# Kernel tuning notes

Measured on AMD Instinct MI355X. Metric: run time of the kernel, lower is better.

Reference implementation:

```python
import jax, jax.numpy as jnp
import numpy as np
import math

DIMS = 128
VOXEL_SIZE = 4.0
QUANT_SIZE = 0.02
QUANT_LEN = int((2 * VOXEL_SIZE + 0.0001) // QUANT_SIZE)  # 400
N = 1024


def setup_inputs() -> dict:
    key = jax.random.key(0)
    k1, k2, k3, k4, k5, k6 = jax.random.split(key, 6)
    features = jax.random.normal(k1, (N, DIMS), dtype=jnp.float32)
    # distances uniform in [-voxel_size, voxel_size)
    voxel_distances = (jax.random.uniform(k2, (N, N, 3), dtype=jnp.float32) * 2.0 - 1.0) * VOXEL_SIZE
    W_qkv = jax.random.normal(k3, (DIMS, 3 * DIMS), dtype=jnp.float32) * 0.02
    b_qkv = jnp.zeros((3 * DIMS,), dtype=jnp.float32)
    table_x = jax.random.normal(k4, (3, QUANT_LEN, DIMS), dtype=jnp.float32) * 0.02
    table_y = jax.random.normal(k5, (3, QUANT_LEN, DIMS), dtype=jnp.float32) * 0.02
    table_z = jax.random.normal(k6, (3, QUANT_LEN, DIMS), dtype=jnp.float32) * 0.02
    return {"features": features, "voxel_distances": voxel_distances,
            "W_qkv": W_qkv, "b_qkv": b_qkv,
            "table_x": table_x, "table_y": table_y, "table_z": table_z}


def reference(features, voxel_distances, W_qkv, b_qkv, table_x, table_y, table_z):
    n, dims = features.shape
    qkv = (features @ W_qkv + b_qkv).reshape(n, 3, dims)
    q, k, v = qkv[:, 0], qkv[:, 1], qkv[:, 2]  # each [N, D]

    # quantized distance indices, clamped like torch's .clamp(max=...)
    max_idx = VOXEL_SIZE * 2.0 / QUANT_SIZE - 1.0  # 399
    idx = jnp.floor((voxel_distances + VOXEL_SIZE) / QUANT_SIZE)
    idx = jnp.clip(idx, 0.0, max_idx).astype(jnp.int32)  # [N, N, 3]

    # gathered positional encoding: [N, N, D]
    encode_k = table_x[1][idx[:, :, 0]] + table_y[1][idx[:, :, 1]] + table_z[1][idx[:, :, 2]]
    # bias[i, j] = k[i] . encode_k[i, j]  (faithful to k[:, None] @ encode_k^T)
    position_bias = jnp.einsum('id,ijd->ij', k, encode_k)

    scores = (q @ k.T + position_bias) / math.sqrt(dims)
    attn = jax.nn.softmax(scores, axis=-1)  # [N, N]
    return attn @ v  # [N, D]
```

## Files before the change

### kernel.cpp

```cpp
#include <hip/hip_runtime.h>
#include <math.h>

#define N_PTS 1024
#define D 128
#define QL 400
#define PLD 1200
#define SQRT_D_INV 0.08838834764831845f

typedef __attribute__((ext_vector_type(8))) short bf16x8;
typedef __attribute__((ext_vector_type(4))) float f32x4;
typedef unsigned short u16;

#define GLOBAL_AS __attribute__((address_space(1)))
#define LDS_AS    __attribute__((address_space(3)))

__device__ __forceinline__ u16 f2bf(float x) {
    union { float f; unsigned u; } v; v.f = x;
    unsigned r = v.u + 0x7fff + ((v.u >> 16) & 1);
    return (u16)(r >> 16);
}
__device__ __forceinline__ float b2f(u16 h) {
    union { unsigned u; float f; } v; v.u = ((unsigned)h) << 16;
    return v.f;
}

__global__ __launch_bounds__(256) void prep_kernel(
    const float* __restrict__ features, const float* __restrict__ W,
    const float* __restrict__ bias,
    const float* __restrict__ tx, const float* __restrict__ ty,
    const float* __restrict__ tz,
    u16* __restrict__ qb, u16* __restrict__ kb, u16* __restrict__ vT,
    u16* __restrict__ Tcat)
{
    __shared__ __align__(16) u16 As[64 * 128];
    __shared__ __align__(16) u16 Bs[64 * 128];
    const int tid = threadIdx.x;
    const int bx = blockIdx.x;

    if (bx >= 96) {
        int e0 = (bx - 96) * 1024 + tid * 4;
        int n = e0 >> 7, k = e0 & 127;
        int sec = n / QL, r = n - sec * QL;
        const float* t = (sec == 0) ? tx : ((sec == 1) ? ty : tz);
        float4 v = *(const float4*)&t[QL * D + r * D + k];
        ushort4 o;
        o.x = f2bf(v.x); o.y = f2bf(v.y); o.z = f2bf(v.z); o.w = f2bf(v.w);
        *(ushort4*)&Tcat[e0] = o;
        return;
    }

    const int wave = tid >> 6, lane = tid & 63;
    const int wr = wave >> 1, wc = wave & 1;
    const int l15 = lane & 15, l4 = lane >> 4;
    const int bm = (bx / 6) * 64;
    const int bn = (bx % 6) * 64;

    #pragma unroll
    for (int r0 = 0; r0 < 4; ++r0) {
        int unit = r0 * 256 + tid;
        int row = unit >> 4, c16 = unit & 15;
        const float* ga = features + (size_t)(bm + row) * D + c16 * 8;
        float4 a0 = *(const float4*)ga;
        float4 a1 = *(const float4*)(ga + 4);
        u16 h[8] = {f2bf(a0.x), f2bf(a0.y), f2bf(a0.z), f2bf(a0.w),
                    f2bf(a1.x), f2bf(a1.y), f2bf(a1.z), f2bf(a1.w)};
        *(bf16x8*)(As + row * 128 + ((c16 ^ (row & 7)) * 8)) = *(bf16x8*)h;
    }
    #pragma unroll
    for (int r2 = 0; r2 < 8; ++r2) {
        int k = r2 * 16 + (tid >> 4);
        int nl = (tid & 15) * 4;
        float4 w4 = *(const float4*)&W[(size_t)k * 384 + bn + nl];
        float wv[4] = {w4.x, w4.y, w4.z, w4.w};
        #pragma unroll
        for (int e = 0; e < 4; ++e) {
            int n = nl + e;
            Bs[n * 128 + ((k >> 3) ^ (n & 7)) * 8 + (k & 7)] = f2bf(wv[e]);
        }
    }
    __syncthreads();

    f32x4 acc[2][2] = {};
    #pragma unroll
    for (int ks = 0; ks < 4; ++ks) {
        bf16x8 a[2], b[2];
        #pragma unroll
        for (int m = 0; m < 2; ++m) {
            int row = wr * 32 + m * 16 + l15;
            int c16 = ks * 4 + l4;
            a[m] = *(const bf16x8*)(As + row * 128 + ((c16 ^ (row & 7)) * 8));
        }
        #pragma unroll
        for (int n = 0; n < 2; ++n) {
            int row = wc * 32 + n * 16 + l15;
            int c16 = ks * 4 + l4;
            b[n] = *(const bf16x8*)(Bs + row * 128 + ((c16 ^ (row & 7)) * 8));
        }
        #pragma unroll
        for (int m = 0; m < 2; ++m)
            #pragma unroll
            for (int n = 0; n < 2; ++n)
                acc[m][n] = __builtin_amdgcn_mfma_f32_16x16x32_bf16(
                    a[m], b[n], acc[m][n], 0, 0, 0);
    }

    #pragma unroll
    for (int m = 0; m < 2; ++m) {
        #pragma unroll
        for (int n = 0; n < 2; ++n) {
            #pragma unroll
            for (int r = 0; r < 4; ++r) {
                int grow = bm + wr * 32 + m * 16 + l4 * 4 + r;
                int gcol = bn + wc * 32 + n * 16 + l15;
                float val = acc[m][n][r] + bias[gcol];
                int reg = gcol >> 7, lc = gcol & 127;
                if (reg == 0)      qb[grow * D + lc] = f2bf(val * SQRT_D_INV);
                else if (reg == 1) kb[grow * D + lc] = f2bf(val);
                else               vT[(size_t)lc * N_PTS + grow] = f2bf(val);
            }
        }
    }
}

__global__ __launch_bounds__(256) void p_gemm_kernel(
    const u16* __restrict__ A,
    const u16* __restrict__ B,
    u16* __restrict__ Cb)
{
    __shared__ __align__(16) u16 As[64 * 128];
    __shared__ __align__(16) u16 Bs[64 * 128];
    const int tid  = threadIdx.x;
    const int wave = tid >> 6, lane = tid & 63;
    const int wr = wave >> 1, wc = wave & 1;
    const int l15 = lane & 15, l4 = lane >> 4;
    const int bm = blockIdx.y * 64, bn = blockIdx.x * 64;

    #pragma unroll
    for (int r = 0; r < 4; ++r) {
        int unit = r * 256 + tid;
        int row  = unit >> 4;
        int c16  = unit & 15;
        int csw  = c16 ^ (row & 7);
        const u16* ga = A + (size_t)(bm + row) * D + csw * 8;
        __builtin_amdgcn_global_load_lds(
            (const GLOBAL_AS unsigned int*)ga,
            (LDS_AS unsigned int*)(As + r * 2048 + wave * 512), 16, 0, 0);
        int brow = bn + row; if (brow > PLD - 1) brow = PLD - 1;
        const u16* gb = B + (size_t)brow * D + csw * 8;
        __builtin_amdgcn_global_load_lds(
            (const GLOBAL_AS unsigned int*)gb,
            (LDS_AS unsigned int*)(Bs + r * 2048 + wave * 512), 16, 0, 0);
    }
    __syncthreads();

    f32x4 acc[2][2] = {};
    #pragma unroll
    for (int ks = 0; ks < 4; ++ks) {
        bf16x8 a[2], b[2];
        #pragma unroll
        for (int m = 0; m < 2; ++m) {
            int row = wr * 32 + m * 16 + l15;
            int c16 = ks * 4 + l4;
            a[m] = *(const bf16x8*)(As + row * 128 + ((c16 ^ (row & 7)) * 8));
        }
        #pragma unroll
        for (int n = 0; n < 2; ++n) {
            int row = wc * 32 + n * 16 + l15;
            int c16 = ks * 4 + l4;
            b[n] = *(const bf16x8*)(Bs + row * 128 + ((c16 ^ (row & 7)) * 8));
        }
        #pragma unroll
        for (int m = 0; m < 2; ++m)
            #pragma unroll
            for (int n = 0; n < 2; ++n)
                acc[m][n] = __builtin_amdgcn_mfma_f32_16x16x32_bf16(
                    a[m], b[n], acc[m][n], 0, 0, 0);
    }

    #pragma unroll
    for (int m = 0; m < 2; ++m)
        #pragma unroll
        for (int n = 0; n < 2; ++n)
            #pragma unroll
            for (int r = 0; r < 4; ++r) {
                int grow = bm + wr * 32 + m * 16 + l4 * 4 + r;
                int gcol = bn + wc * 32 + n * 16 + l15;
                if (gcol < PLD)
                    Cb[(size_t)grow * PLD + gcol] = f2bf(acc[m][n][r] * SQRT_D_INV);
            }
}

__global__ __launch_bounds__(256) void flash_kernel(
    const u16* __restrict__ qb,
    const u16* __restrict__ kb,
    const u16* __restrict__ vT,
    const u16* __restrict__ Pb,
    const float* __restrict__ vd,
    float* __restrict__ part,
    float* __restrict__ rowsumP)
{
    __shared__ __align__(16) u16 Pl[2432 * 8];
    __shared__ __align__(16) u16 Ps[16 * 128];
    __shared__ float rsw[4][16];
    const int tid = threadIdx.x;
    const int wave = tid >> 6, lane = tid & 63;
    const int l15 = lane & 15, l4 = lane >> 4;
    const int bm = blockIdx.y * 16;
    const int bn = blockIdx.x * 128;

    const u16* Pg = Pb + (size_t)bm * PLD;
    #pragma unroll
    for (int r0 = 0; r0 < 9; ++r0) {
        int unit = r0 * 256 + tid;
        __builtin_amdgcn_global_load_lds(
            (const GLOBAL_AS unsigned int*)(Pg + unit * 8),
            (LDS_AS unsigned int*)(Pl + r0 * 2048 + wave * 512), 16, 0, 0);
    }
    if (wave < 2) {
        int unit = 9 * 256 + tid;
        int cu = unit > 2399 ? 2399 : unit;
        __builtin_amdgcn_global_load_lds(
            (const GLOBAL_AS unsigned int*)(Pg + cu * 8),
            (LDS_AS unsigned int*)(Pl + 9 * 2048 + wave * 512), 16, 0, 0);
    }

    float vx[2][4], vy[2][4], vz[2][4];
    #pragma unroll
    for (int nn = 0; nn < 2; ++nn)
        #pragma unroll
        for (int r = 0; r < 4; ++r) {
            int i = l4 * 4 + r;
            int j = wave * 32 + nn * 16 + l15;
            const float* vp = vd + ((size_t)(bm + i) * N_PTS + bn + j) * 3;
            vx[nn][r] = vp[0]; vy[nn][r] = vp[1]; vz[nn][r] = vp[2];
        }

    bf16x8 aq[4];
    #pragma unroll
    for (int ks = 0; ks < 4; ++ks)
        aq[ks] = *(const bf16x8*)(qb + (size_t)(bm + l15) * D + ks * 32 + l4 * 8);
    f32x4 acc[2] = {};
    #pragma unroll
    for (int nn = 0; nn < 2; ++nn) {
        int jt = bn + wave * 32 + nn * 16;
        #pragma unroll
        for (int ks = 0; ks < 4; ++ks) {
            bf16x8 bk = *(const bf16x8*)(kb + (size_t)(jt + l15) * D + ks * 32 + l4 * 8);
            acc[nn] = __builtin_amdgcn_mfma_f32_16x16x32_bf16(aq[ks], bk, acc[nn], 0, 0, 0);
        }
    }
    __syncthreads();

    float rs[4] = {0.f, 0.f, 0.f, 0.f};
    #pragma unroll
    for (int nn = 0; nn < 2; ++nn)
        #pragma unroll
        for (int r = 0; r < 4; ++r) {
            int i = l4 * 4 + r;
            int jl = wave * 32 + nn * 16 + l15;
            int ix = (int)floorf((vx[nn][r] + 4.0f) * 50.0f);
            int iy = (int)floorf((vy[nn][r] + 4.0f) * 50.0f);
            int iz = (int)floorf((vz[nn][r] + 4.0f) * 50.0f);
            ix = min(max(ix, 0), QL - 1);
            iy = min(max(iy, 0), QL - 1);
            iz = min(max(iz, 0), QL - 1);
            const u16* Pr = Pl + i * PLD;
            float bv = b2f(Pr[ix]) + b2f(Pr[QL + iy]) + b2f(Pr[2 * QL + iz]);
            float e = __expf(acc[nn][r] + bv);
            rs[r] += e;
            Ps[i * 128 + (((jl >> 3) ^ (i & 7)) * 8) + (jl & 7)] = f2bf(e);
        }
    #pragma unroll
    for (int r = 0; r < 4; ++r)
        #pragma unroll
        for (int off = 1; off < 16; off <<= 1)
            rs[r] += __shfl_xor(rs[r], off);
    if (l15 == 0)
        #pragma unroll
        for (int r = 0; r < 4; ++r) rsw[wave][l4 * 4 + r] = rs[r];
    __syncthreads();
    if (tid < 16)
        rowsumP[blockIdx.x * N_PTS + bm + tid] =
            rsw[0][tid] + rsw[1][tid] + rsw[2][tid] + rsw[3][tid];

    bf16x8 pa[4];
    #pragma unroll
    for (int kt = 0; kt < 4; ++kt)
        pa[kt] = *(const bf16x8*)(Ps + l15 * 128 + (((kt * 4 + l4) ^ (l15 & 7)) * 8));
    f32x4 acc2[2] = {};
    #pragma unroll
    for (int nn = 0; nn < 2; ++nn) {
        int dt = wave * 32 + nn * 16;
        #pragma unroll
        for (int kt = 0; kt < 4; ++kt) {
            bf16x8 bv8 = *(const bf16x8*)(vT + (size_t)(dt + l15) * N_PTS + bn + kt * 32 + l4 * 8);
            acc2[nn] = __builtin_amdgcn_mfma_f32_16x16x32_bf16(pa[kt], bv8, acc2[nn], 0, 0, 0);
        }
    }
    float* po = part + (size_t)blockIdx.x * (N_PTS * D);
    #pragma unroll
    for (int nn = 0; nn < 2; ++nn)
        #pragma unroll
        for (int r = 0; r < 4; ++r)
            po[(size_t)(bm + l4 * 4 + r) * D + wave * 32 + nn * 16 + l15] = acc2[nn][r];
}

__global__ __launch_bounds__(256) void reduce_norm_kernel(
    const float* __restrict__ part,
    const float* __restrict__ rowsumP,
    float* __restrict__ out)
{
    int e = blockIdx.x * 256 + threadIdx.x;
    int row = e >> 5;
    float rs = 0.0f;
    #pragma unroll
    for (int jb = 0; jb < 8; ++jb) rs += rowsumP[jb * N_PTS + row];
    float inv = 1.0f / rs;
    const float4* p4 = (const float4*)part;
    float4 a = p4[e];
    #pragma unroll
    for (int z = 1; z < 8; ++z) {
        float4 v = p4[(size_t)z * 32768 + e];
        a.x += v.x; a.y += v.y; a.z += v.z; a.w += v.w;
    }
    a.x *= inv; a.y *= inv; a.z *= inv; a.w *= inv;
    ((float4*)out)[e] = a;
}

extern "C" void kernel_launch(void* const* d_in, const int* in_sizes, int n_in,
                              void* d_out, int out_size, void* d_ws, size_t ws_size,
                              hipStream_t stream)
{
    const float* features = (const float*)d_in[0];
    const float* vd       = (const float*)d_in[1];
    const float* W        = (const float*)d_in[2];
    const float* b        = (const float*)d_in[3];
    const float* tx       = (const float*)d_in[4];
    const float* ty       = (const float*)d_in[5];
    const float* tz       = (const float*)d_in[6];
    float* out = (float*)d_out;

    char* w0 = (char*)d_ws;
    u16* qb       = (u16*)w0;
    u16* kb       = (u16*)(w0 + 0x40000);
    u16* vT       = (u16*)(w0 + 0x80000);
    u16* Tcat     = (u16*)(w0 + 0xC0000);
    u16* Pb       = (u16*)(w0 + 0x110000);
    float* part   = (float*)(w0 + 0x370000);
    float* rowsumP= (float*)(w0 + 0x770000);

    dim3 blk(256);

    prep_kernel<<<dim3(246), blk, 0, stream>>>(
        features, W, b, tx, ty, tz, qb, kb, vT, Tcat);

    p_gemm_kernel<<<dim3(19, 16), blk, 0, stream>>>(kb, Tcat, Pb);

    flash_kernel<<<dim3(8, 64), blk, 0, stream>>>(
        qb, kb, vT, Pb, vd, part, rowsumP);

    reduce_norm_kernel<<<dim3(128), blk, 0, stream>>>(part, rowsumP, out);
}
```

Baseline: 29.06 us.

## Fuse QKV projection and positional-table GEMM into one prep kernel

Merges the prep and P-GEMM kernels into one launch. Each P-GEMM block recomputes its 64-row K tile from features and W and converts its slice of the position tables to bf16 itself, so the separate Tcat buffer and one kernel launch go away. Extra blocks compute q/k/v as before. The flash kernel grid is transposed so that consecutive blocks walk rows instead of column chunks. The cost is redundant K-projection work across the 19 column blocks, plus extra LDS traffic for the in-block conversion.

```diff
diff --git a/kernel.cpp b/kernel.cpp
--- a/kernel.cpp
+++ b/kernel.cpp
@@ -24,36 +24,97 @@
     return v.f;
 }
 
-__global__ __launch_bounds__(256) void prep_kernel(
+__global__ __launch_bounds__(256) void prep_all_kernel(
     const float* __restrict__ features, const float* __restrict__ W,
     const float* __restrict__ bias,
     const float* __restrict__ tx, const float* __restrict__ ty,
     const float* __restrict__ tz,
     u16* __restrict__ qb, u16* __restrict__ kb, u16* __restrict__ vT,
-    u16* __restrict__ Tcat)
+    u16* __restrict__ Pb)
 {
-    __shared__ __align__(16) u16 As[64 * 128];
-    __shared__ __align__(16) u16 Bs[64 * 128];
+    __shared__ __align__(16) u16 smem[24576];
+    u16* As = smem;
+    u16* Bs = smem + 8192;
+
     const int tid = threadIdx.x;
     const int bx = blockIdx.x;
-
-    if (bx >= 96) {
-        int e0 = (bx - 96) * 1024 + tid * 4;
-        int n = e0 >> 7, k = e0 & 127;
-        int sec = n / QL, r = n - sec * QL;
-        const float* t = (sec == 0) ? tx : ((sec == 1) ? ty : tz);
-        float4 v = *(const float4*)&t[QL * D + r * D + k];
-        ushort4 o;
-        o.x = f2bf(v.x); o.y = f2bf(v.y); o.z = f2bf(v.z); o.w = f2bf(v.w);
-        *(ushort4*)&Tcat[e0] = o;
-        return;
-    }
-
     const int wave = tid >> 6, lane = tid & 63;
     const int wr = wave >> 1, wc = wave & 1;
     const int l15 = lane & 15, l4 = lane >> 4;
-    const int bm = (bx / 6) * 64;
-    const int bn = (bx % 6) * 64;
+
+    if (bx >= 304) {
+        const int qx = bx - 304;
+        const int bm = (qx / 6) * 64;
+        const int bn = (qx % 6) * 64;
+
+        #pragma unroll
+        for (int r0 = 0; r0 < 4; ++r0) {
+            int unit = r0 * 256 + tid;
+            int row = unit >> 4, c16 = unit & 15;
+            const float* ga = features + (size_t)(bm + row) * D + c16 * 8;
+            float4 a0 = *(const float4*)ga;
+            float4 a1 = *(const float4*)(ga + 4);
+            u16 h[8] = {f2bf(a0.x), f2bf(a0.y), f2bf(a0.z), f2bf(a0.w),
+                        f2bf(a1.x), f2bf(a1.y), f2bf(a1.z), f2bf(a1.w)};
+            *(bf16x8*)(As + row * 128 + ((c16 ^ (row & 7)) * 8)) = *(bf16x8*)h;
+        }
+        #pragma unroll
+        for (int r2 = 0; r2 < 8; ++r2) {
+            int k = r2 * 16 + (tid >> 4);
+            int nl = (tid & 15) * 4;
+            float4 w4 = *(const float4*)&W[(size_t)k * 384 + bn + nl];
+            float wv[4] = {w4.x, w4.y, w4.z, w4.w};
+            #pragma unroll
+            for (int e = 0; e < 4; ++e) {
+                int n = nl + e;
+                Bs[n * 128 + (((k >> 3) ^ (n & 7)) << 3) + (k & 7)] = f2bf(wv[e]);
+            }
+        }
+        __syncthreads();
+
+        f32x4 acc[2][2] = {};
+        #pragma unroll
+        for (int ks = 0; ks < 4; ++ks) {
+            bf16x8 a[2], b[2];
+            #pragma unroll
+            for (int m = 0; m < 2; ++m) {
+                int row = wr * 32 + m * 16 + l15;
+                int c16 = ks * 4 + l4;
+                a[m] = *(const bf16x8*)(As + row * 128 + ((c16 ^ (row & 7)) * 8));
+            }
+            #pragma unroll
+            for (int n = 0; n < 2; ++n) {
+                int row = wc * 32 + n * 16 + l15;
+                int c16 = ks * 4 + l4;
+                b[n] = *(const bf16x8*)(Bs + row * 128 + ((c16 ^ (row & 7)) * 8));
+            }
+            #pragma unroll
+            for (int m = 0; m < 2; ++m)
+                #pragma unroll
+                for (int n = 0; n < 2; ++n)
+                    acc[m][n] = __builtin_amdgcn_mfma_f32_16x16x32_bf16(
+                        a[m], b[n], acc[m][n], 0, 0, 0);
+        }
+
+        #pragma unroll
+        for (int m = 0; m < 2; ++m)
+            #pragma unroll
+            for (int n = 0; n < 2; ++n)
+                #pragma unroll
+                for (int r = 0; r < 4; ++r) {
+                    int grow = bm + wr * 32 + m * 16 + l4 * 4 + r;
+                    int gcol = bn + wc * 32 + n * 16 + l15;
+                    float val = acc[m][n][r] + bias[gcol];
+                    int reg = gcol >> 7, lc = gcol & 127;
+                    if (reg == 0)      qb[grow * D + lc] = f2bf(val * SQRT_D_INV);
+                    else if (reg == 1) kb[grow * D + lc] = f2bf(val);
+                    else               vT[(size_t)lc * N_PTS + grow] = f2bf(val);
+                }
+        return;
+    }
+
+    const int jb = bx % 19, ib = bx / 19;
+    const int bm = ib * 64, bn = jb * 64;
 
     #pragma unroll
     for (int r0 = 0; r0 < 4; ++r0) {
@@ -67,23 +128,23 @@
         *(bf16x8*)(As + row * 128 + ((c16 ^ (row & 7)) * 8)) = *(bf16x8*)h;
     }
     #pragma unroll
-    for (int r2 = 0; r2 < 8; ++r2) {
-        int k = r2 * 16 + (tid >> 4);
-        int nl = (tid & 15) * 4;
-        float4 w4 = *(const float4*)&W[(size_t)k * 384 + bn + nl];
+    for (int r2 = 0; r2 < 16; ++r2) {
+        int kk = r2 * 8 + (tid >> 5);
+        int nl = (tid & 31) * 4;
+        float4 w4 = *(const float4*)&W[(size_t)kk * 384 + 128 + nl];
         float wv[4] = {w4.x, w4.y, w4.z, w4.w};
         #pragma unroll
         for (int e = 0; e < 4; ++e) {
             int n = nl + e;
-            Bs[n * 128 + ((k >> 3) ^ (n & 7)) * 8 + (k & 7)] = f2bf(wv[e]);
-        }
-    }
-    __syncthreads();
-
-    f32x4 acc[2][2] = {};
+            Bs[n * 128 + (((kk >> 3) ^ (n & 7)) << 3) + (kk & 7)] = f2bf(wv[e]);
+        }
+    }
+    __syncthreads();
+
+    f32x4 acc1[2][4] = {};
     #pragma unroll
     for (int ks = 0; ks < 4; ++ks) {
-        bf16x8 a[2], b[2];
+        bf16x8 a[2], b[4];
         #pragma unroll
         for (int m = 0; m < 2; ++m) {
             int row = wr * 32 + m * 16 + l15;
@@ -91,6 +152,57 @@
             a[m] = *(const bf16x8*)(As + row * 128 + ((c16 ^ (row & 7)) * 8));
         }
         #pragma unroll
+        for (int n = 0; n < 4; ++n) {
+            int row = wc * 64 + n * 16 + l15;
+            int c16 = ks * 4 + l4;
+            b[n] = *(const bf16x8*)(Bs + row * 128 + ((c16 ^ (row & 7)) * 8));
+        }
+        #pragma unroll
+        for (int m = 0; m < 2; ++m)
+            #pragma unroll
+            for (int n = 0; n < 4; ++n)
+                acc1[m][n] = __builtin_amdgcn_mfma_f32_16x16x32_bf16(
+                    a[m], b[n], acc1[m][n], 0, 0, 0);
+    }
+    __syncthreads();
+
+    #pragma unroll
+    for (int m = 0; m < 2; ++m)
+        #pragma unroll
+        for (int n = 0; n < 4; ++n)
+            #pragma unroll
+            for (int r = 0; r < 4; ++r) {
+                int lrow = wr * 32 + m * 16 + l4 * 4 + r;
+                int lcol = wc * 64 + n * 16 + l15;
+                float val = acc1[m][n][r] + bias[128 + lcol];
+                As[lrow * 128 + (((lcol >> 3) ^ (lrow & 7)) << 3) + (lcol & 7)] =
+                    f2bf(val);
+            }
+    #pragma unroll
+    for (int r0 = 0; r0 < 8; ++r0) {
+        int e0 = (r0 * 256 + tid) * 4;
+        int trow = e0 >> 7, tcol = e0 & 127;
+        int grow = bn + trow; if (grow > PLD - 1) grow = PLD - 1;
+        int sec = grow / QL, rr = grow - sec * QL;
+        const float* t = (sec == 0) ? tx : ((sec == 1) ? ty : tz);
+        float4 v = *(const float4*)&t[QL * D + rr * D + tcol];
+        u16 h[4] = {f2bf(v.x), f2bf(v.y), f2bf(v.z), f2bf(v.w)};
+        *(ushort4*)(Bs + trow * 128 + (((tcol >> 3) ^ (trow & 7)) << 3) + (tcol & 7))
+            = *(ushort4*)h;
+    }
+    __syncthreads();
+
+    f32x4 acc2[2][2] = {};
+    #pragma unroll
+    for (int ks = 0; ks < 4; ++ks) {
+        bf16x8 a[2], b[2];
+        #pragma unroll
+        for (int m = 0; m < 2; ++m) {
+            int row = wr * 32 + m * 16 + l15;
+            int c16 = ks * 4 + l4;
+            a[m] = *(const bf16x8*)(As + row * 128 + ((c16 ^ (row & 7)) * 8));
+        }
+        #pragma unroll
         for (int n = 0; n < 2; ++n) {
             int row = wc * 32 + n * 16 + l15;
             int c16 = ks * 4 + l4;
@@ -100,83 +212,9 @@
         for (int m = 0; m < 2; ++m)
             #pragma unroll
             for (int n = 0; n < 2; ++n)
-                acc[m][n] = __builtin_amdgcn_mfma_f32_16x16x32_bf16(
-                    a[m], b[n], acc[m][n], 0, 0, 0);
-    }
-
-    #pragma unroll
-    for (int m = 0; m < 2; ++m) {
-        #pragma unroll
-        for (int n = 0; n < 2; ++n) {
-            #pragma unroll
-            for (int r = 0; r < 4; ++r) {
-                int grow = bm + wr * 32 + m * 16 + l4 * 4 + r;
-                int gcol = bn + wc * 32 + n * 16 + l15;
-                float val = acc[m][n][r] + bias[gcol];
-                int reg = gcol >> 7, lc = gcol & 127;
-                if (reg == 0)      qb[grow * D + lc] = f2bf(val * SQRT_D_INV);
-                else if (reg == 1) kb[grow * D + lc] = f2bf(val);
-                else               vT[(size_t)lc * N_PTS + grow] = f2bf(val);
-            }
-        }
-    }
-}
-
-__global__ __launch_bounds__(256) void p_gemm_kernel(
-    const u16* __restrict__ A,
-    const u16* __restrict__ B,
-    u16* __restrict__ Cb)
-{
-    __shared__ __align__(16) u16 As[64 * 128];
-    __shared__ __align__(16) u16 Bs[64 * 128];
-    const int tid  = threadIdx.x;
-    const int wave = tid >> 6, lane = tid & 63;
-    const int wr = wave >> 1, wc = wave & 1;
-    const int l15 = lane & 15, l4 = lane >> 4;
-    const int bm = blockIdx.y * 64, bn = blockIdx.x * 64;
-
-    #pragma unroll
-    for (int r = 0; r < 4; ++r) {
-        int unit = r * 256 + tid;
-        int row  = unit >> 4;
-        int c16  = unit & 15;
-        int csw  = c16 ^ (row & 7);
-        const u16* ga = A + (size_t)(bm + row) * D + csw * 8;
-        __builtin_amdgcn_global_load_lds(
-            (const GLOBAL_AS unsigned int*)ga,
-            (LDS_AS unsigned int*)(As + r * 2048 + wave * 512), 16, 0, 0);
-        int brow = bn + row; if (brow > PLD - 1) brow = PLD - 1;
-        const u16* gb = B + (size_t)brow * D + csw * 8;
-        __builtin_amdgcn_global_load_lds(
-            (const GLOBAL_AS unsigned int*)gb,
-            (LDS_AS unsigned int*)(Bs + r * 2048 + wave * 512), 16, 0, 0);
-    }
-    __syncthreads();
-
-    f32x4 acc[2][2] = {};
-    #pragma unroll
-    for (int ks = 0; ks < 4; ++ks) {
-        bf16x8 a[2], b[2];
-        #pragma unroll
-        for (int m = 0; m < 2; ++m) {
-            int row = wr * 32 + m * 16 + l15;
-            int c16 = ks * 4 + l4;
-            a[m] = *(const bf16x8*)(As + row * 128 + ((c16 ^ (row & 7)) * 8));
-        }
-        #pragma unroll
-        for (int n = 0; n < 2; ++n) {
-            int row = wc * 32 + n * 16 + l15;
-            int c16 = ks * 4 + l4;
-            b[n] = *(const bf16x8*)(Bs + row * 128 + ((c16 ^ (row & 7)) * 8));
-        }
-        #pragma unroll
-        for (int m = 0; m < 2; ++m)
-            #pragma unroll
-            for (int n = 0; n < 2; ++n)
-                acc[m][n] = __builtin_amdgcn_mfma_f32_16x16x32_bf16(
-                    a[m], b[n], acc[m][n], 0, 0, 0);
-    }
-
+                acc2[m][n] = __builtin_amdgcn_mfma_f32_16x16x32_bf16(
+                    a[m], b[n], acc2[m][n], 0, 0, 0);
+    }
     #pragma unroll
     for (int m = 0; m < 2; ++m)
         #pragma unroll
@@ -186,7 +224,7 @@
                 int grow = bm + wr * 32 + m * 16 + l4 * 4 + r;
                 int gcol = bn + wc * 32 + n * 16 + l15;
                 if (gcol < PLD)
-                    Cb[(size_t)grow * PLD + gcol] = f2bf(acc[m][n][r] * SQRT_D_INV);
+                    Pb[(size_t)grow * PLD + gcol] = f2bf(acc2[m][n][r] * SQRT_D_INV);
             }
 }
 
@@ -205,8 +243,9 @@
     const int tid = threadIdx.x;
     const int wave = tid >> 6, lane = tid & 63;
     const int l15 = lane & 15, l4 = lane >> 4;
-    const int bm = blockIdx.y * 16;
-    const int bn = blockIdx.x * 128;
+    const int bm = blockIdx.x * 16;
+    const int bn = blockIdx.y * 128;
+    const int chunk = blockIdx.y;
 
     const u16* Pg = Pb + (size_t)bm * PLD;
     #pragma unroll
@@ -280,7 +319,7 @@
         for (int r = 0; r < 4; ++r) rsw[wave][l4 * 4 + r] = rs[r];
     __syncthreads();
     if (tid < 16)
-        rowsumP[blockIdx.x * N_PTS + bm + tid] =
+        rowsumP[chunk * N_PTS + bm + tid] =
             rsw[0][tid] + rsw[1][tid] + rsw[2][tid] + rsw[3][tid];
 
     bf16x8 pa[4];
@@ -297,7 +336,7 @@
             acc2[nn] = __builtin_amdgcn_mfma_f32_16x16x32_bf16(pa[kt], bv8, acc2[nn], 0, 0, 0);
         }
     }
-    float* po = part + (size_t)blockIdx.x * (N_PTS * D);
+    float* po = part + (size_t)chunk * (N_PTS * D);
     #pragma unroll
     for (int nn = 0; nn < 2; ++nn)
         #pragma unroll
@@ -344,19 +383,16 @@
     u16* qb       = (u16*)w0;
     u16* kb       = (u16*)(w0 + 0x40000);
     u16* vT       = (u16*)(w0 + 0x80000);
-    u16* Tcat     = (u16*)(w0 + 0xC0000);
-    u16* Pb       = (u16*)(w0 + 0x110000);
-    float* part   = (float*)(w0 + 0x370000);
-    float* rowsumP= (float*)(w0 + 0x770000);
+    u16* Pb       = (u16*)(w0 + 0xC0000);
+    float* part   = (float*)(w0 + 0x320000);
+    float* rowsumP= (float*)(w0 + 0x720000);
 
     dim3 blk(256);
 
-    prep_kernel<<<dim3(246), blk, 0, stream>>>(
-        features, W, b, tx, ty, tz, qb, kb, vT, Tcat);
-
-    p_gemm_kernel<<<dim3(19, 16), blk, 0, stream>>>(kb, Tcat, Pb);
-
-    flash_kernel<<<dim3(8, 64), blk, 0, stream>>>(
+    prep_all_kernel<<<dim3(400), blk, 0, stream>>>(
+        features, W, b, tx, ty, tz, qb, kb, vT, Pb);
+
+    flash_kernel<<<dim3(64, 8), blk, 0, stream>>>(
         qb, kb, vT, Pb, vd, part, rowsumP);
 
     reduce_norm_kernel<<<dim3(128), blk, 0, stream>>>(part, rowsumP, out);
```

Result: slower. 29.79 us (+2.5%).

## Fuse four kernels into one persistent kernel with software grid barriers

Applied to the files above, without the earlier changes.

Merges the prep, P-GEMM, flash attention and reduce kernels into a single 256-block persistent kernel. A global atomic-counter barrier separates the stages, and the barrier counter is cleared with a memset before launch. This is meant to remove the launch gaps and tails between the four kernels. In exchange, each block does more serial work (two column chunks per flash tile, a strided loop over the P-GEMM tiles), the reduce stage only uses 128 threads per block, and correctness relies on all 256 blocks being resident at once.

```diff
diff --git a/kernel.cpp b/kernel.cpp
--- a/kernel.cpp
+++ b/kernel.cpp
@@ -6,6 +6,7 @@
 #define QL 400
 #define PLD 1200
 #define SQRT_D_INV 0.08838834764831845f
+#define NB 256
 
 typedef __attribute__((ext_vector_type(8))) short bf16x8;
 typedef __attribute__((ext_vector_type(4))) float f32x4;
@@ -24,20 +25,112 @@
     return v.f;
 }
 
-__global__ __launch_bounds__(256) void prep_kernel(
+__device__ __forceinline__ void grid_bar(unsigned* cnt, int epoch) {
+    __syncthreads();
+    if (threadIdx.x == 0) {
+        __threadfence();
+        __hip_atomic_fetch_add(cnt, 1u, __ATOMIC_RELAXED, __HIP_MEMORY_SCOPE_AGENT);
+        const unsigned target = (unsigned)epoch * NB;
+        int guard = 0;
+        while (__hip_atomic_load(cnt, __ATOMIC_RELAXED, __HIP_MEMORY_SCOPE_AGENT) < target) {
+            __builtin_amdgcn_s_sleep(2);
+            if (++guard > (1 << 24)) break;
+        }
+        __threadfence();
+    }
+    __syncthreads();
+}
+
+__global__ __launch_bounds__(256, 2) void mega_kernel(
     const float* __restrict__ features, const float* __restrict__ W,
     const float* __restrict__ bias,
     const float* __restrict__ tx, const float* __restrict__ ty,
     const float* __restrict__ tz,
+    const float* __restrict__ vd,
     u16* __restrict__ qb, u16* __restrict__ kb, u16* __restrict__ vT,
-    u16* __restrict__ Tcat)
+    u16* __restrict__ Tcat, u16* __restrict__ Pb,
+    float* __restrict__ part, float* __restrict__ rowsumP,
+    float* __restrict__ out, unsigned* __restrict__ barcnt)
 {
-    __shared__ __align__(16) u16 As[64 * 128];
-    __shared__ __align__(16) u16 Bs[64 * 128];
+    __shared__ __align__(16) char smem_raw[43520];
+    u16* As = (u16*)smem_raw;
+    u16* Bs = As + 8192;
+    u16* Pl = (u16*)smem_raw;
+    u16* Ps = (u16*)(smem_raw + 38912);
+    float* rsw = (float*)(smem_raw + 43008);
+
     const int tid = threadIdx.x;
     const int bx = blockIdx.x;
-
-    if (bx >= 96) {
+    const int wave = tid >> 6, lane = tid & 63;
+    const int wr = wave >> 1, wc = wave & 1;
+    const int l15 = lane & 15, l4 = lane >> 4;
+
+    if (bx < 96) {
+        const int bm = (bx / 6) * 64;
+        const int bn = (bx % 6) * 64;
+        #pragma unroll
+        for (int r0 = 0; r0 < 4; ++r0) {
+            int unit = r0 * 256 + tid;
+            int row = unit >> 4, c16 = unit & 15;
+            const float* ga = features + (size_t)(bm + row) * D + c16 * 8;
+            float4 a0 = *(const float4*)ga;
+            float4 a1 = *(const float4*)(ga + 4);
+            u16 h[8] = {f2bf(a0.x), f2bf(a0.y), f2bf(a0.z), f2bf(a0.w),
+                        f2bf(a1.x), f2bf(a1.y), f2bf(a1.z), f2bf(a1.w)};
+            *(bf16x8*)(As + row * 128 + ((c16 ^ (row & 7)) * 8)) = *(bf16x8*)h;
+        }
+        #pragma unroll
+        for (int r2 = 0; r2 < 8; ++r2) {
+            int k = r2 * 16 + (tid >> 4);
+            int nl = (tid & 15) * 4;
+            float4 w4 = *(const float4*)&W[(size_t)k * 384 + bn + nl];
+            float wv[4] = {w4.x, w4.y, w4.z, w4.w};
+            #pragma unroll
+            for (int e = 0; e < 4; ++e) {
+                int n = nl + e;
+                Bs[n * 128 + (((k >> 3) ^ (n & 7)) << 3) + (k & 7)] = f2bf(wv[e]);
+            }
+        }
+        __syncthreads();
+
+        f32x4 acc[2][2] = {};
+        #pragma unroll
+        for (int ks = 0; ks < 4; ++ks) {
+            bf16x8 a[2], b[2];
+            #pragma unroll
+            for (int m = 0; m < 2; ++m) {
+                int row = wr * 32 + m * 16 + l15;
+                int c16 = ks * 4 + l4;
+                a[m] = *(const bf16x8*)(As + row * 128 + ((c16 ^ (row & 7)) * 8));
+            }
+            #pragma unroll
+            for (int n = 0; n < 2; ++n) {
+                int row = wc * 32 + n * 16 + l15;
+                int c16 = ks * 4 + l4;
+                b[n] = *(const bf16x8*)(Bs + row * 128 + ((c16 ^ (row & 7)) * 8));
+            }
+            #pragma unroll
+            for (int m = 0; m < 2; ++m)
+                #pragma unroll
+                for (int n = 0; n < 2; ++n)
+                    acc[m][n] = __builtin_amdgcn_mfma_f32_16x16x32_bf16(
+                        a[m], b[n], acc[m][n], 0, 0, 0);
+        }
+        #pragma unroll
+        for (int m = 0; m < 2; ++m)
+            #pragma unroll
+            for (int n = 0; n < 2; ++n)
+                #pragma unroll
+                for (int r = 0; r < 4; ++r) {
+                    int grow = bm + wr * 32 + m * 16 + l4 * 4 + r;
+                    int gcol = bn + wc * 32 + n * 16 + l15;
+                    float val = acc[m][n][r] + bias[gcol];
+                    int reg = gcol >> 7, lc = gcol & 127;
+                    if (reg == 0)      qb[grow * D + lc] = f2bf(val * SQRT_D_INV);
+                    else if (reg == 1) kb[grow * D + lc] = f2bf(val);
+                    else               vT[(size_t)lc * N_PTS + grow] = f2bf(val);
+                }
+    } else if (bx < 246) {
         int e0 = (bx - 96) * 1024 + tid * 4;
         int n = e0 >> 7, k = e0 & 127;
         int sec = n / QL, r = n - sec * QL;
@@ -46,285 +139,197 @@
         ushort4 o;
         o.x = f2bf(v.x); o.y = f2bf(v.y); o.z = f2bf(v.z); o.w = f2bf(v.w);
         *(ushort4*)&Tcat[e0] = o;
-        return;
-    }
-
-    const int wave = tid >> 6, lane = tid & 63;
-    const int wr = wave >> 1, wc = wave & 1;
-    const int l15 = lane & 15, l4 = lane >> 4;
-    const int bm = (bx / 6) * 64;
-    const int bn = (bx % 6) * 64;
-
-    #pragma unroll
-    for (int r0 = 0; r0 < 4; ++r0) {
-        int unit = r0 * 256 + tid;
-        int row = unit >> 4, c16 = unit & 15;
-        const float* ga = features + (size_t)(bm + row) * D + c16 * 8;
-        float4 a0 = *(const float4*)ga;
-        float4 a1 = *(const float4*)(ga + 4);
-        u16 h[8] = {f2bf(a0.x), f2bf(a0.y), f2bf(a0.z), f2bf(a0.w),
-                    f2bf(a1.x), f2bf(a1.y), f2bf(a1.z), f2bf(a1.w)};
-        *(bf16x8*)(As + row * 128 + ((c16 ^ (row & 7)) * 8)) = *(bf16x8*)h;
-    }
-    #pragma unroll
-    for (int r2 = 0; r2 < 8; ++r2) {
-        int k = r2 * 16 + (tid >> 4);
-        int nl = (tid & 15) * 4;
-        float4 w4 = *(const float4*)&W[(size_t)k * 384 + bn + nl];
-        float wv[4] = {w4.x, w4.y, w4.z, w4.w};
-        #pragma unroll
-        for (int e = 0; e < 4; ++e) {
-            int n = nl + e;
-            Bs[n * 128 + ((k >> 3) ^ (n & 7)) * 8 + (k & 7)] = f2bf(wv[e]);
-        }
-    }
-    __syncthreads();
-
-    f32x4 acc[2][2] = {};
-    #pragma unroll
-    for (int ks = 0; ks < 4; ++ks) {
-        bf16x8 a[2], b[2];
-        #pragma unroll
-        for (int m = 0; m < 2; ++m) {
-            int row = wr * 32 + m * 16 + l15;
-            int c16 = ks * 4 + l4;
-            a[m] = *(const bf16x8*)(As + row * 128 + ((c16 ^ (row & 7)) * 8));
-        }
-        #pragma unroll
-        for (int n = 0; n < 2; ++n) {
-            int row = wc * 32 + n * 16 + l15;
-            int c16 = ks * 4 + l4;
-            b[n] = *(const bf16x8*)(Bs + row * 128 + ((c16 ^ (row & 7)) * 8));
+    }
+
+    grid_bar(barcnt, 1);
+
+    for (int t = bx; t < 304; t += NB) {
+        __syncthreads();
+        const int bm = (t / 19) * 64, bn = (t % 19) * 64;
+        #pragma unroll
+        for (int r = 0; r < 4; ++r) {
+            int unit = r * 256 + tid;
+            int row  = unit >> 4;
+            int c16  = unit & 15;
+            int csw  = c16 ^ (row & 7);
+            const u16* ga = kb + (size_t)(bm + row) * D + csw * 8;
+            __builtin_amdgcn_global_load_lds(
+                (const GLOBAL_AS unsigned int*)ga,
+                (LDS_AS unsigned int*)(As + r * 2048 + wave * 512), 16, 0, 0);
+            int brow = bn + row; if (brow > PLD - 1) brow = PLD - 1;
+            const u16* gb = Tcat + (size_t)brow * D + csw * 8;
+            __builtin_amdgcn_global_load_lds(
+                (const GLOBAL_AS unsigned int*)gb,
+                (LDS_AS unsigned int*)(Bs + r * 2048 + wave * 512), 16, 0, 0);
+        }
+        __syncthreads();
+
+        f32x4 acc[2][2] = {};
+        #pragma unroll
+        for (int ks = 0; ks < 4; ++ks) {
+            bf16x8 a[2], b[2];
+            #pragma unroll
+            for (int m = 0; m < 2; ++m) {
+                int row = wr * 32 + m * 16 + l15;
+                int c16 = ks * 4 + l4;
+                a[m] = *(const bf16x8*)(As + row * 128 + ((c16 ^ (row & 7)) * 8));
+            }
+            #pragma unroll
+            for (int n = 0; n < 2; ++n) {
+                int row = wc * 32 + n * 16 + l15;
+                int c16 = ks * 4 + l4;
+                b[n] = *(const bf16x8*)(Bs + row * 128 + ((c16 ^ (row & 7)) * 8));
+            }
+            #pragma unroll
+            for (int m = 0; m < 2; ++m)
+                #pragma unroll
+                for (int n = 0; n < 2; ++n)
+                    acc[m][n] = __builtin_amdgcn_mfma_f32_16x16x32_bf16(
+                        a[m], b[n], acc[m][n], 0, 0, 0);
         }
         #pragma unroll
         for (int m = 0; m < 2; ++m)
             #pragma unroll
             for (int n = 0; n < 2; ++n)
-                acc[m][n] = __builtin_amdgcn_mfma_f32_16x16x32_bf16(
-                    a[m], b[n], acc[m][n], 0, 0, 0);
-    }
-
-    #pragma unroll
-    for (int m = 0; m < 2; ++m) {
-        #pragma unroll
-        for (int n = 0; n < 2; ++n) {
-            #pragma unroll
-            for (int r = 0; r < 4; ++r) {
-                int grow = bm + wr * 32 + m * 16 + l4 * 4 + r;
-                int gcol = bn + wc * 32 + n * 16 + l15;
-                float val = acc[m][n][r] + bias[gcol];
-                int reg = gcol >> 7, lc = gcol & 127;
-                if (reg == 0)      qb[grow * D + lc] = f2bf(val * SQRT_D_INV);
-                else if (reg == 1) kb[grow * D + lc] = f2bf(val);
-                else               vT[(size_t)lc * N_PTS + grow] = f2bf(val);
-            }
-        }
-    }
-}
-
-__global__ __launch_bounds__(256) void p_gemm_kernel(
-    const u16* __restrict__ A,
-    const u16* __restrict__ B,
-    u16* __restrict__ Cb)
-{
-    __shared__ __align__(16) u16 As[64 * 128];
-    __shared__ __align__(16) u16 Bs[64 * 128];
-    const int tid  = threadIdx.x;
-    const int wave = tid >> 6, lane = tid & 63;
-    const int wr = wave >> 1, wc = wave & 1;
-    const int l15 = lane & 15, l4 = lane >> 4;
-    const int bm = blockIdx.y * 64, bn = blockIdx.x * 64;
-
-    #pragma unroll
-    for (int r = 0; r < 4; ++r) {
-        int unit = r * 256 + tid;
-        int row  = unit >> 4;
-        int c16  = unit & 15;
-        int csw  = c16 ^ (row & 7);
-        const u16* ga = A + (size_t)(bm + row) * D + csw * 8;
-        __builtin_amdgcn_global_load_lds(
-            (const GLOBAL_AS unsigned int*)ga,
-            (LDS_AS unsigned int*)(As + r * 2048 + wave * 512), 16, 0, 0);
-        int brow = bn + row; if (brow > PLD - 1) brow = PLD - 1;
-        const u16* gb = B + (size_t)brow * D + csw * 8;
-        __builtin_amdgcn_global_load_lds(
-            (const GLOBAL_AS unsigned int*)gb,
-            (LDS_AS unsigned int*)(Bs + r * 2048 + wave * 512), 16, 0, 0);
-    }
-    __syncthreads();
-
-    f32x4 acc[2][2] = {};
-    #pragma unroll
-    for (int ks = 0; ks < 4; ++ks) {
-        bf16x8 a[2], b[2];
-        #pragma unroll
-        for (int m = 0; m < 2; ++m) {
-            int row = wr * 32 + m * 16 + l15;
-            int c16 = ks * 4 + l4;
-            a[m] = *(const bf16x8*)(As + row * 128 + ((c16 ^ (row & 7)) * 8));
-        }
-        #pragma unroll
-        for (int n = 0; n < 2; ++n) {
-            int row = wc * 32 + n * 16 + l15;
-            int c16 = ks * 4 + l4;
-            b[n] = *(const bf16x8*)(Bs + row * 128 + ((c16 ^ (row & 7)) * 8));
-        }
-        #pragma unroll
-        for (int m = 0; m < 2; ++m)
-            #pragma unroll
-            for (int n = 0; n < 2; ++n)
-                acc[m][n] = __builtin_amdgcn_mfma_f32_16x16x32_bf16(
-                    a[m], b[n], acc[m][n], 0, 0, 0);
-    }
-
-    #pragma unroll
-    for (int m = 0; m < 2; ++m)
-        #pragma unroll
-        for (int n = 0; n < 2; ++n)
-            #pragma unroll
-            for (int r = 0; r < 4; ++r) {
-                int grow = bm + wr * 32 + m * 16 + l4 * 4 + r;
-                int gcol = bn + wc * 32 + n * 16 + l15;
-                if (gcol < PLD)
-                    Cb[(size_t)grow * PLD + gcol] = f2bf(acc[m][n][r] * SQRT_D_INV);
-            }
-}
-
-__global__ __launch_bounds__(256) void flash_kernel(
-    const u16* __restrict__ qb,
-    const u16* __restrict__ kb,
-    const u16* __restrict__ vT,
-    const u16* __restrict__ Pb,
-    const float* __restrict__ vd,
-    float* __restrict__ part,
-    float* __restrict__ rowsumP)
-{
-    __shared__ __align__(16) u16 Pl[2432 * 8];
-    __shared__ __align__(16) u16 Ps[16 * 128];
-    __shared__ float rsw[4][16];
-    const int tid = threadIdx.x;
-    const int wave = tid >> 6, lane = tid & 63;
-    const int l15 = lane & 15, l4 = lane >> 4;
-    const int bm = blockIdx.y * 16;
-    const int bn = blockIdx.x * 128;
-
-    const u16* Pg = Pb + (size_t)bm * PLD;
-    #pragma unroll
-    for (int r0 = 0; r0 < 9; ++r0) {
-        int unit = r0 * 256 + tid;
-        __builtin_amdgcn_global_load_lds(
-            (const GLOBAL_AS unsigned int*)(Pg + unit * 8),
-            (LDS_AS unsigned int*)(Pl + r0 * 2048 + wave * 512), 16, 0, 0);
-    }
-    if (wave < 2) {
-        int unit = 9 * 256 + tid;
-        int cu = unit > 2399 ? 2399 : unit;
-        __builtin_amdgcn_global_load_lds(
-            (const GLOBAL_AS unsigned int*)(Pg + cu * 8),
-            (LDS_AS unsigned int*)(Pl + 9 * 2048 + wave * 512), 16, 0, 0);
-    }
-
-    float vx[2][4], vy[2][4], vz[2][4];
-    #pragma unroll
-    for (int nn = 0; nn < 2; ++nn)
-        #pragma unroll
-        for (int r = 0; r < 4; ++r) {
-            int i = l4 * 4 + r;
-            int j = wave * 32 + nn * 16 + l15;
-            const float* vp = vd + ((size_t)(bm + i) * N_PTS + bn + j) * 3;
-            vx[nn][r] = vp[0]; vy[nn][r] = vp[1]; vz[nn][r] = vp[2];
-        }
-
-    bf16x8 aq[4];
-    #pragma unroll
-    for (int ks = 0; ks < 4; ++ks)
-        aq[ks] = *(const bf16x8*)(qb + (size_t)(bm + l15) * D + ks * 32 + l4 * 8);
-    f32x4 acc[2] = {};
-    #pragma unroll
-    for (int nn = 0; nn < 2; ++nn) {
-        int jt = bn + wave * 32 + nn * 16;
-        #pragma unroll
-        for (int ks = 0; ks < 4; ++ks) {
-            bf16x8 bk = *(const bf16x8*)(kb + (size_t)(jt + l15) * D + ks * 32 + l4 * 8);
-            acc[nn] = __builtin_amdgcn_mfma_f32_16x16x32_bf16(aq[ks], bk, acc[nn], 0, 0, 0);
-        }
-    }
-    __syncthreads();
-
-    float rs[4] = {0.f, 0.f, 0.f, 0.f};
-    #pragma unroll
-    for (int nn = 0; nn < 2; ++nn)
-        #pragma unroll
-        for (int r = 0; r < 4; ++r) {
-            int i = l4 * 4 + r;
-            int jl = wave * 32 + nn * 16 + l15;
-            int ix = (int)floorf((vx[nn][r] + 4.0f) * 50.0f);
-            int iy = (int)floorf((vy[nn][r] + 4.0f) * 50.0f);
-            int iz = (int)floorf((vz[nn][r] + 4.0f) * 50.0f);
-            ix = min(max(ix, 0), QL - 1);
-            iy = min(max(iy, 0), QL - 1);
-            iz = min(max(iz, 0), QL - 1);
-            const u16* Pr = Pl + i * PLD;
-            float bv = b2f(Pr[ix]) + b2f(Pr[QL + iy]) + b2f(Pr[2 * QL + iz]);
-            float e = __expf(acc[nn][r] + bv);
-            rs[r] += e;
-            Ps[i * 128 + (((jl >> 3) ^ (i & 7)) * 8) + (jl & 7)] = f2bf(e);
-        }
-    #pragma unroll
-    for (int r = 0; r < 4; ++r)
-        #pragma unroll
-        for (int off = 1; off < 16; off <<= 1)
-            rs[r] += __shfl_xor(rs[r], off);
-    if (l15 == 0)
-        #pragma unroll
-        for (int r = 0; r < 4; ++r) rsw[wave][l4 * 4 + r] = rs[r];
-    __syncthreads();
-    if (tid < 16)
-        rowsumP[blockIdx.x * N_PTS + bm + tid] =
-            rsw[0][tid] + rsw[1][tid] + rsw[2][tid] + rsw[3][tid];
-
-    bf16x8 pa[4];
-    #pragma unroll
-    for (int kt = 0; kt < 4; ++kt)
-        pa[kt] = *(const bf16x8*)(Ps + l15 * 128 + (((kt * 4 + l4) ^ (l15 & 7)) * 8));
-    f32x4 acc2[2] = {};
-    #pragma unroll
-    for (int nn = 0; nn < 2; ++nn) {
-        int dt = wave * 32 + nn * 16;
-        #pragma unroll
-        for (int kt = 0; kt < 4; ++kt) {
-            bf16x8 bv8 = *(const bf16x8*)(vT + (size_t)(dt + l15) * N_PTS + bn + kt * 32 + l4 * 8);
-            acc2[nn] = __builtin_amdgcn_mfma_f32_16x16x32_bf16(pa[kt], bv8, acc2[nn], 0, 0, 0);
-        }
-    }
-    float* po = part + (size_t)blockIdx.x * (N_PTS * D);
-    #pragma unroll
-    for (int nn = 0; nn < 2; ++nn)
-        #pragma unroll
-        for (int r = 0; r < 4; ++r)
-            po[(size_t)(bm + l4 * 4 + r) * D + wave * 32 + nn * 16 + l15] = acc2[nn][r];
-}
-
-__global__ __launch_bounds__(256) void reduce_norm_kernel(
-    const float* __restrict__ part,
-    const float* __restrict__ rowsumP,
-    float* __restrict__ out)
-{
-    int e = blockIdx.x * 256 + threadIdx.x;
-    int row = e >> 5;
-    float rs = 0.0f;
-    #pragma unroll
-    for (int jb = 0; jb < 8; ++jb) rs += rowsumP[jb * N_PTS + row];
-    float inv = 1.0f / rs;
-    const float4* p4 = (const float4*)part;
-    float4 a = p4[e];
-    #pragma unroll
-    for (int z = 1; z < 8; ++z) {
-        float4 v = p4[(size_t)z * 32768 + e];
-        a.x += v.x; a.y += v.y; a.z += v.z; a.w += v.w;
-    }
-    a.x *= inv; a.y *= inv; a.z *= inv; a.w *= inv;
-    ((float4*)out)[e] = a;
+                #pragma unroll
+                for (int r = 0; r < 4; ++r) {
+                    int grow = bm + wr * 32 + m * 16 + l4 * 4 + r;
+                    int gcol = bn + wc * 32 + n * 16 + l15;
+                    if (gcol < PLD)
+                        Pb[(size_t)grow * PLD + gcol] = f2bf(acc[m][n][r] * SQRT_D_INV);
+                }
+    }
+
+    grid_bar(barcnt, 2);
+
+    {
+        const int bi = bx >> 2;
+        const int cp = bx & 3;
+        const int bm = bi * 16;
+
+        const u16* Pg = Pb + (size_t)bm * PLD;
+        #pragma unroll
+        for (int r0 = 0; r0 < 9; ++r0) {
+            int unit = r0 * 256 + tid;
+            __builtin_amdgcn_global_load_lds(
+                (const GLOBAL_AS unsigned int*)(Pg + unit * 8),
+                (LDS_AS unsigned int*)(Pl + r0 * 2048 + wave * 512), 16, 0, 0);
+        }
+        if (wave < 2) {
+            int unit = 9 * 256 + tid;
+            int cu = unit > 2399 ? 2399 : unit;
+            __builtin_amdgcn_global_load_lds(
+                (const GLOBAL_AS unsigned int*)(Pg + cu * 8),
+                (LDS_AS unsigned int*)(Pl + 9 * 2048 + wave * 512), 16, 0, 0);
+        }
+
+        bf16x8 aq[4];
+        #pragma unroll
+        for (int ks = 0; ks < 4; ++ks)
+            aq[ks] = *(const bf16x8*)(qb + (size_t)(bm + l15) * D + ks * 32 + l4 * 8);
+
+        for (int cc = 0; cc < 2; ++cc) {
+            const int chunk = cp * 2 + cc;
+            const int bn = chunk * 128;
+
+            float vx[2][4], vy[2][4], vz[2][4];
+            #pragma unroll
+            for (int nn = 0; nn < 2; ++nn)
+                #pragma unroll
+                for (int r = 0; r < 4; ++r) {
+                    int i = l4 * 4 + r;
+                    int j = wave * 32 + nn * 16 + l15;
+                    const float* vp = vd + ((size_t)(bm + i) * N_PTS + bn + j) * 3;
+                    vx[nn][r] = vp[0]; vy[nn][r] = vp[1]; vz[nn][r] = vp[2];
+                }
+
+            f32x4 acc[2] = {};
+            #pragma unroll
+            for (int nn = 0; nn < 2; ++nn) {
+                int jt = bn + wave * 32 + nn * 16;
+                #pragma unroll
+                for (int ks = 0; ks < 4; ++ks) {
+                    bf16x8 bk = *(const bf16x8*)(kb + (size_t)(jt + l15) * D + ks * 32 + l4 * 8);
+                    acc[nn] = __builtin_amdgcn_mfma_f32_16x16x32_bf16(aq[ks], bk, acc[nn], 0, 0, 0);
+                }
+            }
+            __syncthreads();
+
+            float rs[4] = {0.f, 0.f, 0.f, 0.f};
+            #pragma unroll
+            for (int nn = 0; nn < 2; ++nn)
+                #pragma unroll
+                for (int r = 0; r < 4; ++r) {
+                    int i = l4 * 4 + r;
+                    int jl = wave * 32 + nn * 16 + l15;
+                    int ix = (int)floorf((vx[nn][r] + 4.0f) * 50.0f);
+                    int iy = (int)floorf((vy[nn][r] + 4.0f) * 50.0f);
+                    int iz = (int)floorf((vz[nn][r] + 4.0f) * 50.0f);
+                    ix = min(max(ix, 0), QL - 1);
+                    iy = min(max(iy, 0), QL - 1);
+                    iz = min(max(iz, 0), QL - 1);
+                    const u16* Pr = Pl + i * PLD;
+                    float bv = b2f(Pr[ix]) + b2f(Pr[QL + iy]) + b2f(Pr[2 * QL + iz]);
+                    float e = __expf(acc[nn][r] + bv);
+                    rs[r] += e;
+                    Ps[i * 128 + (((jl >> 3) ^ (i & 7)) * 8) + (jl & 7)] = f2bf(e);
+                }
+            #pragma unroll
+            for (int r = 0; r < 4; ++r)
+                #pragma unroll
+                for (int off = 1; off < 16; off <<= 1)
+                    rs[r] += __shfl_xor(rs[r], off);
+            if (l15 == 0)
+                #pragma unroll
+                for (int r = 0; r < 4; ++r) rsw[wave * 16 + l4 * 4 + r] = rs[r];
+            __syncthreads();
+            if (tid < 16)
+                rowsumP[chunk * N_PTS + bm + tid] =
+                    rsw[tid] + rsw[16 + tid] + rsw[32 + tid] + rsw[48 + tid];
+
+            bf16x8 pa[4];
+            #pragma unroll
+            for (int kt = 0; kt < 4; ++kt)
+                pa[kt] = *(const bf16x8*)(Ps + l15 * 128 + (((kt * 4 + l4) ^ (l15 & 7)) * 8));
+            f32x4 acc2[2] = {};
+            #pragma unroll
+            for (int nn = 0; nn < 2; ++nn) {
+                int dt = wave * 32 + nn * 16;
+                #pragma unroll
+                for (int kt = 0; kt < 4; ++kt) {
+                    bf16x8 bv8 = *(const bf16x8*)(vT + (size_t)(dt + l15) * N_PTS + bn + kt * 32 + l4 * 8);
+                    acc2[nn] = __builtin_amdgcn_mfma_f32_16x16x32_bf16(pa[kt], bv8, acc2[nn], 0, 0, 0);
+                }
+            }
+            float* po = part + (size_t)chunk * (N_PTS * D);
+            #pragma unroll
+            for (int nn = 0; nn < 2; ++nn)
+                #pragma unroll
+                for (int r = 0; r < 4; ++r)
+                    po[(size_t)(bm + l4 * 4 + r) * D + wave * 32 + nn * 16 + l15] = acc2[nn][r];
+            __syncthreads();
+        }
+    }
+
+    grid_bar(barcnt, 3);
+
+    if (tid < 128) {
+        int e = bx * 128 + tid;
+        int row = e >> 5;
+        float rsum = 0.0f;
+        #pragma unroll
+        for (int jb = 0; jb < 8; ++jb) rsum += rowsumP[jb * N_PTS + row];
+        float inv = 1.0f / rsum;
+        const float4* p4 = (const float4*)part;
+        float4 a = p4[e];
+        #pragma unroll
+        for (int z = 1; z < 8; ++z) {
+            float4 v = p4[(size_t)z * 32768 + e];
+            a.x += v.x; a.y += v.y; a.z += v.z; a.w += v.w;
+        }
+        a.x *= inv; a.y *= inv; a.z *= inv; a.w *= inv;
+        ((float4*)out)[e] = a;
+    }
 }
 
 extern "C" void kernel_launch(void* const* d_in, const int* in_sizes, int n_in,
@@ -341,23 +346,18 @@
     float* out = (float*)d_out;
 
     char* w0 = (char*)d_ws;
-    u16* qb       = (u16*)w0;
-    u16* kb       = (u16*)(w0 + 0x40000);
-    u16* vT       = (u16*)(w0 + 0x80000);
-    u16* Tcat     = (u16*)(w0 + 0xC0000);
-    u16* Pb       = (u16*)(w0 + 0x110000);
-    float* part   = (float*)(w0 + 0x370000);
-    float* rowsumP= (float*)(w0 + 0x770000);
-
-    dim3 blk(256);
-
-    prep_kernel<<<dim3(246), blk, 0, stream>>>(
-        features, W, b, tx, ty, tz, qb, kb, vT, Tcat);
-
-    p_gemm_kernel<<<dim3(19, 16), blk, 0, stream>>>(kb, Tcat, Pb);
-
-    flash_kernel<<<dim3(8, 64), blk, 0, stream>>>(
-        qb, kb, vT, Pb, vd, part, rowsumP);
-
-    reduce_norm_kernel<<<dim3(128), blk, 0, stream>>>(part, rowsumP, out);
-}
+    unsigned* barcnt = (unsigned*)w0;
+    u16* qb       = (u16*)(w0 + 0x1000);
+    u16* kb       = (u16*)(w0 + 0x50000);
+    u16* vT       = (u16*)(w0 + 0x90000);
+    u16* Tcat     = (u16*)(w0 + 0xD0000);
+    u16* Pb       = (u16*)(w0 + 0x120000);
+    float* part   = (float*)(w0 + 0x380000);
+    float* rowsumP= (float*)(w0 + 0x780000);
+
+    hipMemsetAsync(barcnt, 0, 64, stream);
+
+    mega_kernel<<<dim3(NB), dim3(256), 0, stream>>>(
+        features, W, b, tx, ty, tz, vd,
+        qb, kb, vT, Tcat, Pb, part, rowsumP, out, barcnt);
+}
```

After: 98.95 us. 241% more time.
